# Kernel tuning notes

Hardware: AMD Instinct MI355X
Metric: run time of the kernel (lower is better)

Reference implementation:

```python
import jax, jax.numpy as jnp
import numpy as np

N_NODES = 100_000
N_EDGES = 3_200_000
NR = 10_000
NRHO = 10_000
CUTOFF = 6.0
RHO_MAX = 60.0


def natural_cubic_coeffs(x, y):
    """Natural cubic spline coefficients. x:[K], y:[K,C] -> a,b,c,d each [K-1,C]."""
    K, C = y.shape
    h = np.diff(x)
    rhs = 6.0 * ((y[2:] - y[1:-1]) / h[1:, None] - (y[1:-1] - y[:-2]) / h[:-1, None])
    n = K - 2
    diag = 2.0 * (h[:-1] + h[1:])
    off = h[1:-1]
    # Thomas algorithm for the tridiagonal system (natural BC: M[0]=M[K-1]=0)
    cp = np.zeros(n)
    dp = np.zeros((n, C))
    cp[0] = off[0] / diag[0] if n > 1 else 0.0
    dp[0] = rhs[0] / diag[0]
    for i in range(1, n):
        denom = diag[i] - off[i - 1] * cp[i - 1]
        if i < n - 1:
            cp[i] = off[i] / denom
        dp[i] = (rhs[i] - off[i - 1] * dp[i - 1]) / denom
    M = np.zeros((K, C))
    M[n] = dp[n - 1]
    for i in range(n - 2, -1, -1):
        M[i + 1] = dp[i] - cp[i] * M[i + 2]
    a = y[:-1]
    b = (y[1:] - y[:-1]) / h[:, None] - h[:, None] * (2.0 * M[:-1] + M[1:]) / 6.0
    c = M[:-1] / 2.0
    d = (M[1:] - M[:-1]) / (6.0 * h[:, None])
    f32 = lambda z: jnp.asarray(z, dtype=jnp.float32)
    return f32(a), f32(b), f32(c), f32(d)


def spline_eval(x, knots, a, b, c, d):
    """Piecewise cubic eval. x:[M], knots:[K], coeffs:[K-1,C] -> [M,C]."""
    idx = jnp.clip(jnp.searchsorted(knots, x, side='right') - 1, 0, knots.shape[0] - 2)
    s = (x - knots[idx])[:, None]  # offset within segment
    return a[idx] + s * (b[idx] + s * (c[idx] + s * d[idx]))


def setup_inputs() -> dict:
    key = jax.random.key(0)
    k1, k2, k3 = jax.random.split(key, 3)
    # edge displacement vectors; norms ~ chi(3)*1.2, well within cutoff
    r = jax.random.normal(k1, (N_EDGES, 3), dtype=jnp.float32) * 1.2
    src = jax.random.randint(k2, (N_EDGES,), 0, N_NODES, dtype=jnp.int32)
    dst = jax.random.randint(k3, (N_EDGES,), 0, N_NODES, dtype=jnp.int32)
    # synthetic smooth setfl tables (density, r*phi, embedding)
    rs = np.linspace(0.0, CUTOFF, NR)
    rhos_g = np.linspace(0.0, RHO_MAX, NRHO)
    density = np.exp(-rs)
    rphi = 27.2 * 0.529 * np.exp(-2.0 * rs) * (1.0 + 2.0 * rs)
    embedded = -np.sqrt(rhos_g) + 0.05 * rhos_g
    rad_a, rad_b, rad_c, rad_d = natural_cubic_coeffs(rs, np.stack([density, rphi], axis=1))
    emb_a, emb_b, emb_c, emb_d = natural_cubic_coeffs(rhos_g, embedded[:, None])
    return dict(
        r=r, src=src, dst=dst, n_nodes=N_NODES,
        rs=jnp.asarray(rs, jnp.float32), rhos=jnp.asarray(rhos_g, jnp.float32),
        rad_a=rad_a, rad_b=rad_b, rad_c=rad_c, rad_d=rad_d,
        emb_a=emb_a, emb_b=emb_b, emb_c=emb_c, emb_d=emb_d,
    )


def reference(r, src, dst, n_nodes, rs, rhos, rad_a, rad_b, rad_c, rad_d,
              emb_a, emb_b, emb_c, emb_d):
    def energy(r_):
        bl = jnp.linalg.norm(r_, axis=1)                       # [E]
        rp = spline_eval(bl, rs, rad_a, rad_b, rad_c, rad_d)   # [E,2]
        rho_e = rp[:, 0]
        phi_e = rp[:, 1] / bl                                  # rphi / r
        node_rho = jax.ops.segment_sum(rho_e, dst, num_segments=n_nodes)  # [N]
        F = spline_eval(node_rho, rhos, emb_a, emb_b, emb_c, emb_d)[:, 0]
        return jnp.sum(F) + 0.5 * jnp.sum(phi_e)

    E, dEdr = jax.value_and_grad(energy)(r)
    # r_ij = x_dst - x_src  =>  F_k = sum_{src=k} dE/dr - sum_{dst=k} dE/dr
    forces = (jax.ops.segment_sum(dEdr, src, num_segments=n_nodes)
              - jax.ops.segment_sum(dEdr, dst, num_segments=n_nodes))
    return E, forces
```

## Files before the change

### kernel.cpp

```cpp
#include <hip/hip_runtime.h>
#include <math.h>


static constexpr int SHIFT_P = 12;
static constexpr int NPP     = 4096;
static constexpr int PMAX    = 32;
static constexpr int GSTRIDE = 32;
static constexpr int KR      = 8;
static constexpr int KB      = 16;
static constexpr int CH1     = 4096;
static constexpr int CH3     = 2048;

static constexpr float QSCALE = 524288.0f;
static constexpr float QSTEP  = 1.0f / QSCALE;
static constexpr float FSCALE = 1024.0f;
static constexpr float FSTEP  = 1.0f / FSCALE;

__device__ __forceinline__ double block_reduce_d(double v) {
    #pragma unroll
    for (int off = 32; off > 0; off >>= 1)
        v += __shfl_down(v, off, 64);
    __shared__ double smem[16];
    const int lane = threadIdx.x & 63;
    const int wave = threadIdx.x >> 6;
    if (threadIdx.x < 16) smem[threadIdx.x] = 0.0;
    __syncthreads();
    if (lane == 0) smem[wave] = v;
    __syncthreads();
    if (wave == 0) {
        v = (lane < 16) ? smem[lane] : 0.0;
        #pragma unroll
        for (int off = 8; off > 0; off >>= 1)
            v += __shfl_down(v, off, 64);
    }
    return v;
}

__device__ __forceinline__ int clamp_idx(int i, int hi) {
    return i < 0 ? 0 : (i > hi ? hi : i);
}

__device__ __forceinline__ unsigned f2bf(float f) {
    unsigned u = __float_as_uint(f);
    return (u + 0x7FFFu + ((u >> 16) & 1u)) >> 16;
}
__device__ __forceinline__ float bf2f_hi(unsigned w) { return __uint_as_float(w & 0xFFFF0000u); }
__device__ __forceinline__ float bf2f_lo(unsigned w) { return __uint_as_float(w << 16); }
__device__ __forceinline__ unsigned fq(float f) {
    float s = f * FSCALE;
    s = fminf(fmaxf(s, -1.0e9f), 1.0e9f);
    return (unsigned)(int)rintf(s);
}

__global__ void eam_prep(
    const float* __restrict__ rad_a, const float* __restrict__ rad_b,
    const float* __restrict__ rad_c, const float* __restrict__ rad_d,
    const float* __restrict__ ea, const float* __restrict__ eb,
    const float* __restrict__ ec, const float* __restrict__ ed,
    float4* __restrict__ pack8, float4* __restrict__ pack4,
    int* __restrict__ gCur, int nr1, int nrho1)
{
    const int i = blockIdx.x * 256 + threadIdx.x;
    if (i < 2 * PMAX * GSTRIDE) gCur[i] = 0;
    if (i < nr1) {
        pack8[2*i]   = make_float4(rad_a[2*i], rad_a[2*i+1], rad_b[2*i], rad_b[2*i+1]);
        pack8[2*i+1] = make_float4(rad_c[2*i], rad_c[2*i+1], rad_d[2*i], rad_d[2*i+1]);
    }
    if (i < nrho1)
        pack4[i] = make_float4(ea[i], eb[i], ec[i], ed[i]);
}


__global__ void __launch_bounds__(512) eam_p1a(
    const float* __restrict__ r, const int* __restrict__ dst,
    const float4* __restrict__ pack8,
    unsigned* __restrict__ recR, int* __restrict__ gCurR, double* __restrict__ p1,
    float2* __restrict__ ebuf,
    int n_edges, float inv_h, float h, int kmax, int P, int capR)
{
    __shared__ int hist[PMAX], base[PMAX], cur[PMAX], gbase[PMAX];
    __shared__ int tot;
    __shared__ unsigned buf[CH1];
    __shared__ unsigned char pbk[CH1];
    const int tid = threadIdx.x;
    const int e0 = blockIdx.x * CH1;
    const int e1 = min(e0 + CH1, n_edges);
    double phi = 0.0;
    unsigned rec[8]; int pk[8]; bool val[8];
    if (tid < P) hist[tid] = 0;
    __syncthreads();
    #pragma unroll
    for (int k = 0; k < 8; ++k) {
        const int e = e0 + k * 512 + tid;
        val[k] = e < e1;
        rec[k] = 0; pk[k] = 0;
        if (val[k]) {
            const float x = r[3*e], y = r[3*e+1], z = r[3*e+2];
            const float bl = sqrtf(x*x + y*y + z*z);
            int idx = (int)(bl * inv_h); idx = idx > kmax ? kmax : idx;
            const float s = bl - (float)idx * h;
            const float4 q0 = pack8[2*idx];
            const float4 q1 = pack8[2*idx + 1];
            const float rho  = q0.x + s*(q0.z + s*(q1.x + s*q1.z));
            const float rphi = q0.y + s*(q0.w + s*(q1.y + s*q1.w));
            phi += 0.5 * (double)(rphi / bl);
            const float drho  = q0.z + s*(2.0f*q1.x + 3.0f*q1.z*s);
            const float drphi = q0.w + s*(2.0f*q1.y + 3.0f*q1.w*s);
            const float inv_bl = 1.0f / bl;
            const float dphi = (drphi - rphi * inv_bl) * inv_bl;
            ebuf[e] = make_float2(drho, dphi);
            const int node = dst[e];
            pk[k] = node >> SHIFT_P;
            int q = (int)(rho * QSCALE + 0.5f);
            q = q < 0 ? 0 : (q > 0xFFFFF ? 0xFFFFF : q);
            rec[k] = ((unsigned)(node & (NPP - 1)) << 20) | (unsigned)q;
            atomicAdd(&hist[pk[k]], 1);
        }
    }
    __syncthreads();
    if (tid < 64) {
        const int lane = tid;
        const int hv = (lane < P) ? hist[lane] : 0;
        int s = hv;
        #pragma unroll
        for (int off = 1; off < 32; off <<= 1) {
            const int t = __shfl_up(s, off, 64);
            if (lane >= off) s += t;
        }
        if (lane < P) {
            base[lane] = s - hv;
            cur[lane]  = s - hv;
            gbase[lane] = hv ? atomicAdd(&gCurR[lane * GSTRIDE], hv) : 0;
        }
        if (lane == P - 1) tot = s;
    }
    __syncthreads();
    #pragma unroll
    for (int k = 0; k < 8; ++k) {
        if (val[k]) {
            const int pos = atomicAdd(&cur[pk[k]], 1);
            buf[pos] = rec[k];
            pbk[pos] = (unsigned char)pk[k];
        }
    }
    __syncthreads();
    const int T = tot;
    for (int i = tid; i < T; i += 512) {
        const int pp = pbk[i];
        const int gi = gbase[pp] + (i - base[pp]);
        if (gi < capR) recR[(size_t)pp * capR + gi] = buf[i];
    }
    const double bs = block_reduce_d(phi);
    if (tid == 0) p1[blockIdx.x] = bs;
}

__global__ void __launch_bounds__(512) eam_p1b(
    const unsigned* __restrict__ recR, const int* __restrict__ gCurR,
    float* __restrict__ partR, int capR)
{
    __shared__ unsigned acc[NPP];
    const int tid = threadIdx.x;
    const int p = blockIdx.x / KR, j = blockIdx.x % KR;
    for (int i = tid; i < NPP; i += 512) acc[i] = 0u;
    __syncthreads();
    int cnt = gCurR[p * GSTRIDE]; cnt = cnt > capR ? capR : cnt;
    const int per = (((cnt + KR - 1) / KR) + 3) & ~3;
    const int lo = j * per, hi = min(lo + per, cnt);
    const unsigned* seg = recR + (size_t)p * capR;
    int i = lo + 4 * tid;
    for (; i + 4 * 512 + 3 < hi; i += 2 * 4 * 512) {
        const uint4 a = *(const uint4*)(seg + i);
        const uint4 b = *(const uint4*)(seg + i + 4 * 512);
        atomicAdd(&acc[a.x >> 20], a.x & 0xFFFFFu);
        atomicAdd(&acc[a.y >> 20], a.y & 0xFFFFFu);
        atomicAdd(&acc[a.z >> 20], a.z & 0xFFFFFu);
        atomicAdd(&acc[a.w >> 20], a.w & 0xFFFFFu);
        atomicAdd(&acc[b.x >> 20], b.x & 0xFFFFFu);
        atomicAdd(&acc[b.y >> 20], b.y & 0xFFFFFu);
        atomicAdd(&acc[b.z >> 20], b.z & 0xFFFFFu);
        atomicAdd(&acc[b.w >> 20], b.w & 0xFFFFFu);
    }
    for (; i + 3 < hi; i += 4 * 512) {
        const uint4 a = *(const uint4*)(seg + i);
        atomicAdd(&acc[a.x >> 20], a.x & 0xFFFFFu);
        atomicAdd(&acc[a.y >> 20], a.y & 0xFFFFFu);
        atomicAdd(&acc[a.z >> 20], a.z & 0xFFFFFu);
        atomicAdd(&acc[a.w >> 20], a.w & 0xFFFFFu);
    }
    for (int t = (hi & ~3) + tid; t < hi; t += 512) {
        const unsigned w = seg[t];
        atomicAdd(&acc[w >> 20], w & 0xFFFFFu);
    }
    __syncthreads();
    float* out = partR + (size_t)blockIdx.x * NPP;
    for (int k = tid; k < NPP; k += 512) out[k] = (float)acc[k] * QSTEP;
}

__global__ void __launch_bounds__(1024) eam_p1c(
    const float* __restrict__ partR, const float4* __restrict__ pack4,
    float* __restrict__ Fp, double* __restrict__ p2,
    int n_nodes, float inv_h, float h, int kmax)
{
    const int n = blockIdx.x * 1024 + threadIdx.x;
    double fsum = 0.0;
    if (n < n_nodes) {
        const int p = n >> SHIFT_P, l = n & (NPP - 1);
        float rho = 0.0f;
        #pragma unroll
        for (int j = 0; j < KR; ++j)
            rho += partR[(size_t)(p * KR + j) * NPP + l];
        int idx = clamp_idx((int)(rho * inv_h), kmax);
        const float s = rho - (float)idx * h;
        const float4 q = pack4[idx];
        fsum = (double)(q.x + s*(q.y + s*(q.z + s*q.w)));
        Fp[n] = q.y + s*(2.0f*q.z + 3.0f*q.w*s);
    }
    const double bs = block_reduce_d(fsum);
    if (threadIdx.x == 0) p2[blockIdx.x] = bs;
}


__global__ void __launch_bounds__(512) eam_p3a(
    const float* __restrict__ r, const int* __restrict__ src, const int* __restrict__ dst,
    const float2* __restrict__ ebuf, const float* __restrict__ Fp,
    int2* __restrict__ recF, int* __restrict__ gCurF,
    int n_edges, int P, int capF)
{
    __shared__ int hist[PMAX], base[PMAX], cur[PMAX], gbase[PMAX];
    __shared__ int tot;
    __shared__ int2 buf[2 * CH3];
    __shared__ unsigned char pbk[2 * CH3];
    const int tid = threadIdx.x;
    const int e0 = blockIdx.x * CH3;
    const int e1 = min(e0 + CH3, n_edges);
    int2 sa[4], da[4]; int ps[4], pd[4]; bool val[4];
    if (tid < P) hist[tid] = 0;
    __syncthreads();
    #pragma unroll
    for (int k = 0; k < 4; ++k) {
        const int e = e0 + k * 512 + tid;
        val[k] = e < e1;
        ps[k] = pd[k] = 0;
        sa[k] = da[k] = make_int2(0, 0);
        if (val[k]) {
            const float x = r[3*e], y = r[3*e+1], z = r[3*e+2];
            const float bl = sqrtf(x*x + y*y + z*z);
            const float inv_bl = 1.0f / bl;
            const float2 dd = ebuf[e];
            const int si = src[e], di = dst[e];
            const float g = Fp[di] * dd.x + 0.5f * dd.y;
            const float coef = g * inv_bl;
            const unsigned bx = f2bf(coef * x), by = f2bf(coef * y), bz = f2bf(coef * z);
            ps[k] = si >> SHIFT_P;
            pd[k] = di >> SHIFT_P;
            sa[k] = make_int2((int)(((unsigned)(si & (NPP-1)) << 16) | bx),
                              (int)((by << 16) | bz));
            da[k] = make_int2((int)(((unsigned)(di & (NPP-1)) << 16) | (bx ^ 0x8000u)),
                              (int)(((by ^ 0x8000u) << 16) | (bz ^ 0x8000u)));
            atomicAdd(&hist[ps[k]], 1);
            atomicAdd(&hist[pd[k]], 1);
        }
    }
    __syncthreads();
    if (tid < 64) {
        const int lane = tid;
        const int hv = (lane < P) ? hist[lane] : 0;
        int s = hv;
        #pragma unroll
        for (int off = 1; off < 32; off <<= 1) {
            const int t = __shfl_up(s, off, 64);
            if (lane >= off) s += t;
        }
        if (lane < P) {
            base[lane] = s - hv;
            cur[lane]  = s - hv;
            gbase[lane] = hv ? atomicAdd(&gCurF[lane * GSTRIDE], hv) : 0;
        }
        if (lane == P - 1) tot = s;
    }
    __syncthreads();
    #pragma unroll
    for (int k = 0; k < 4; ++k) {
        if (val[k]) {
            int pos = atomicAdd(&cur[ps[k]], 1);
            buf[pos] = sa[k];
            pbk[pos] = (unsigned char)ps[k];
            pos = atomicAdd(&cur[pd[k]], 1);
            buf[pos] = da[k];
            pbk[pos] = (unsigned char)pd[k];
        }
    }
    __syncthreads();
    const int T = tot;
    for (int i = tid; i < T; i += 512) {
        const int pp = pbk[i];
        const int gi = gbase[pp] + (i - base[pp]);
        if (gi < capF) recF[(size_t)pp * capF + gi] = buf[i];
    }
}

__global__ void __launch_bounds__(512) eam_p3b(
    const int2* __restrict__ recF, const int* __restrict__ gCurF,
    int* __restrict__ partF, int capF)
{
    __shared__ unsigned acc[NPP * 3];
    const int tid = threadIdx.x;
    const int p = blockIdx.x / KB, j = blockIdx.x % KB;
    for (int i = tid; i < NPP * 3; i += 512) acc[i] = 0u;
    __syncthreads();
    int cnt = gCurF[p * GSTRIDE]; cnt = cnt > capF ? capF : cnt;
    const int per = (((cnt + KB - 1) / KB) + 3) & ~3;
    const int lo = j * per, hi = min(lo + per, cnt);
    const int2* seg = recF + (size_t)p * capF;
    int i = lo + 2 * tid;
    for (; i + 6 * 512 + 1 < hi; i += 8 * 512) {
        const uint4 a = *(const uint4*)(seg + i);
        const uint4 b = *(const uint4*)(seg + i + 2 * 512);
        const uint4 c = *(const uint4*)(seg + i + 4 * 512);
        const uint4 d = *(const uint4*)(seg + i + 6 * 512);
        int li;
        li = (int)(a.x >> 16) * 3;
        atomicAdd(&acc[li+0], fq(bf2f_lo(a.x))); atomicAdd(&acc[li+1], fq(bf2f_hi(a.y))); atomicAdd(&acc[li+2], fq(bf2f_lo(a.y)));
        li = (int)(a.z >> 16) * 3;
        atomicAdd(&acc[li+0], fq(bf2f_lo(a.z))); atomicAdd(&acc[li+1], fq(bf2f_hi(a.w))); atomicAdd(&acc[li+2], fq(bf2f_lo(a.w)));
        li = (int)(b.x >> 16) * 3;
        atomicAdd(&acc[li+0], fq(bf2f_lo(b.x))); atomicAdd(&acc[li+1], fq(bf2f_hi(b.y))); atomicAdd(&acc[li+2], fq(bf2f_lo(b.y)));
        li = (int)(b.z >> 16) * 3;
        atomicAdd(&acc[li+0], fq(bf2f_lo(b.z))); atomicAdd(&acc[li+1], fq(bf2f_hi(b.w))); atomicAdd(&acc[li+2], fq(bf2f_lo(b.w)));
        li = (int)(c.x >> 16) * 3;
        atomicAdd(&acc[li+0], fq(bf2f_lo(c.x))); atomicAdd(&acc[li+1], fq(bf2f_hi(c.y))); atomicAdd(&acc[li+2], fq(bf2f_lo(c.y)));
        li = (int)(c.z >> 16) * 3;
        atomicAdd(&acc[li+0], fq(bf2f_lo(c.z))); atomicAdd(&acc[li+1], fq(bf2f_hi(c.w))); atomicAdd(&acc[li+2], fq(bf2f_lo(c.w)));
        li = (int)(d.x >> 16) * 3;
        atomicAdd(&acc[li+0], fq(bf2f_lo(d.x))); atomicAdd(&acc[li+1], fq(bf2f_hi(d.y))); atomicAdd(&acc[li+2], fq(bf2f_lo(d.y)));
        li = (int)(d.z >> 16) * 3;
        atomicAdd(&acc[li+0], fq(bf2f_lo(d.z))); atomicAdd(&acc[li+1], fq(bf2f_hi(d.w))); atomicAdd(&acc[li+2], fq(bf2f_lo(d.w)));
    }
    for (; i + 1 < hi; i += 2 * 512) {
        const uint4 a = *(const uint4*)(seg + i);
        int li = (int)(a.x >> 16) * 3;
        atomicAdd(&acc[li+0], fq(bf2f_lo(a.x))); atomicAdd(&acc[li+1], fq(bf2f_hi(a.y))); atomicAdd(&acc[li+2], fq(bf2f_lo(a.y)));
        li = (int)(a.z >> 16) * 3;
        atomicAdd(&acc[li+0], fq(bf2f_lo(a.z))); atomicAdd(&acc[li+1], fq(bf2f_hi(a.w))); atomicAdd(&acc[li+2], fq(bf2f_lo(a.w)));
    }
    for (int t = (hi & ~1) + tid; t < hi; t += 512) {
        const int2 rc = seg[t];
        const unsigned w0 = (unsigned)rc.x, w1 = (unsigned)rc.y;
        const int li = (int)(w0 >> 16) * 3;
        atomicAdd(&acc[li+0], fq(bf2f_lo(w0)));
        atomicAdd(&acc[li+1], fq(bf2f_hi(w1)));
        atomicAdd(&acc[li+2], fq(bf2f_lo(w1)));
    }
    __syncthreads();
    int* out = partF + (size_t)blockIdx.x * (NPP * 3);
    for (int k = tid; k < NPP * 3; k += 512) out[k] = (int)acc[k];
}

__global__ void __launch_bounds__(1024) eam_p3c(
    const int* __restrict__ partF, float* __restrict__ outF, int n_nodes)
{
    const int g = blockIdx.x * 1024 + threadIdx.x;
    if (g >= 3 * n_nodes) return;
    const int n = g / 3, c = g - 3 * n;
    const int p = n >> SHIFT_P, l = n & (NPP - 1);
    int v = 0;
    #pragma unroll
    for (int j = 0; j < KB; ++j)
        v += partF[(size_t)(p * KB + j) * (NPP * 3) + l * 3 + c];
    outF[g] = (float)v * FSTEP;
}

__global__ void __launch_bounds__(256) eam_final_e(
    const double* __restrict__ p1, int n1,
    const double* __restrict__ p2, int n2,
    float* __restrict__ outE)
{
    double v = 0.0;
    for (int i = threadIdx.x; i < n1; i += 256) v += p1[i];
    for (int i = threadIdx.x; i < n2; i += 256) v += p2[i];
    const double bs = block_reduce_d(v);
    if (threadIdx.x == 0) *outE = (float)bs;
}


__global__ void __launch_bounds__(256) eam_pass1(
    const float* __restrict__ r, const int* __restrict__ dst,
    const float* __restrict__ rs,
    const float* __restrict__ rad_a, const float* __restrict__ rad_b,
    const float* __restrict__ rad_c, const float* __restrict__ rad_d,
    float* __restrict__ node_rho, double* __restrict__ p1,
    int n_edges, float inv_h, int kmax)
{
    const int e = blockIdx.x * 256 + threadIdx.x;
    double phi_half = 0.0;
    if (e < n_edges) {
        const float x = r[3*e], y = r[3*e+1], z = r[3*e+2];
        const float bl = sqrtf(x*x + y*y + z*z);
        const int idx = clamp_idx((int)(bl * inv_h), kmax);
        const float s = bl - rs[idx];
        const float a0 = rad_a[2*idx], a1 = rad_a[2*idx+1];
        const float b0 = rad_b[2*idx], b1 = rad_b[2*idx+1];
        const float c0 = rad_c[2*idx], c1 = rad_c[2*idx+1];
        const float d0 = rad_d[2*idx], d1 = rad_d[2*idx+1];
        const float rho  = a0 + s*(b0 + s*(c0 + s*d0));
        const float rphi = a1 + s*(b1 + s*(c1 + s*d1));
        unsafeAtomicAdd(&node_rho[dst[e]], rho);
        phi_half = 0.5 * (double)(rphi / bl);
    }
    const double bs = block_reduce_d(phi_half);
    if (threadIdx.x == 0) p1[blockIdx.x] = bs;
}

__global__ void __launch_bounds__(256) eam_pass2(
    const float* __restrict__ node_rho, const float* __restrict__ rhos,
    const float* __restrict__ ea, const float* __restrict__ eb,
    const float* __restrict__ ec, const float* __restrict__ ed,
    float* __restrict__ Fp, double* __restrict__ p2,
    int n_nodes, float inv_h, int kmax)
{
    const int n = blockIdx.x * 256 + threadIdx.x;
    double fsum = 0.0;
    if (n < n_nodes) {
        const float rho = node_rho[n];
        const int idx = clamp_idx((int)(rho * inv_h), kmax);
        const float s = rho - rhos[idx];
        const float A = ea[idx], B = eb[idx], C = ec[idx], D = ed[idx];
        fsum = (double)(A + s*(B + s*(C + s*D)));
        Fp[n] = B + s*(2.0f*C + 3.0f*D*s);
    }
    const double bs = block_reduce_d(fsum);
    if (threadIdx.x == 0) p2[blockIdx.x] = bs;
}

__global__ void __launch_bounds__(256) eam_pass3(
    const float* __restrict__ r, const int* __restrict__ src,
    const int* __restrict__ dst, const float* __restrict__ rs,
    const float* __restrict__ rad_a, const float* __restrict__ rad_b,
    const float* __restrict__ rad_c, const float* __restrict__ rad_d,
    const float* __restrict__ Fp, float* __restrict__ forces,
    int n_edges, float inv_h, int kmax)
{
    const int e = blockIdx.x * 256 + threadIdx.x;
    if (e >= n_edges) return;
    const float x = r[3*e], y = r[3*e+1], z = r[3*e+2];
    const float bl = sqrtf(x*x + y*y + z*z);
    const int idx = clamp_idx((int)(bl * inv_h), kmax);
    const float s = bl - rs[idx];
    const float a1 = rad_a[2*idx+1];
    const float b0 = rad_b[2*idx], b1 = rad_b[2*idx+1];
    const float c0 = rad_c[2*idx], c1 = rad_c[2*idx+1];
    const float d0 = rad_d[2*idx], d1 = rad_d[2*idx+1];
    const float drho  = b0 + s*(2.0f*c0 + 3.0f*d0*s);
    const float rphi  = a1 + s*(b1 + s*(c1 + s*d1));
    const float drphi = b1 + s*(2.0f*c1 + 3.0f*d1*s);
    const float inv_bl = 1.0f / bl;
    const float dphi = (drphi - rphi*inv_bl) * inv_bl;
    const int si = src[e], di = dst[e];
    const float g = Fp[di]*drho + 0.5f*dphi;
    const float coef = g * inv_bl;
    const float fx = coef*x, fy = coef*y, fz = coef*z;
    unsafeAtomicAdd(&forces[3*si+0], fx);
    unsafeAtomicAdd(&forces[3*si+1], fy);
    unsafeAtomicAdd(&forces[3*si+2], fz);
    unsafeAtomicAdd(&forces[3*di+0], -fx);
    unsafeAtomicAdd(&forces[3*di+1], -fy);
    unsafeAtomicAdd(&forces[3*di+2], -fz);
}


extern "C" void kernel_launch(void* const* d_in, const int* in_sizes, int n_in,
                              void* d_out, int out_size, void* d_ws, size_t ws_size,
                              hipStream_t stream) {
    const float* r     = (const float*)d_in[0];
    const int*   src   = (const int*)d_in[1];
    const int*   dst   = (const int*)d_in[2];
    const float* rs    = (const float*)d_in[4];
    const float* rhos  = (const float*)d_in[5];
    const float* rad_a = (const float*)d_in[6];
    const float* rad_b = (const float*)d_in[7];
    const float* rad_c = (const float*)d_in[8];
    const float* rad_d = (const float*)d_in[9];
    const float* ea    = (const float*)d_in[10];
    const float* eb    = (const float*)d_in[11];
    const float* ec    = (const float*)d_in[12];
    const float* ed    = (const float*)d_in[13];

    const int n_edges = in_sizes[0] / 3;
    const int n_nodes = (out_size - 1) / 3;
    const int nr      = in_sizes[4];
    const int nrho    = in_sizes[5];

    float* outE = (float*)d_out;
    float* outF = (float*)d_out + 1;

    const float inv_hr   = (float)((double)(nr - 1) / 6.0);
    const float hr       = (float)(6.0 / (double)(nr - 1));
    const float inv_hrho = (float)((double)(nrho - 1) / 60.0);
    const float hrho     = (float)(60.0 / (double)(nrho - 1));

    auto al = [](size_t x) { return (x + 255) & ~(size_t)255; };
    char* ws = (char*)d_ws;

    const int P    = (n_nodes + NPP - 1) >> SHIFT_P;
    const int nb1a = (n_edges + CH1 - 1) / CH1;
    const int nb3a = (n_edges + CH3 - 1) / CH3;
    const int nb1c = (n_nodes + 1023) / 1024;
    const int nb3c = (3 * n_nodes + 1023) / 1024;
    const int capR = (n_edges / P + n_edges / (8 * P) + 2048) & ~3;
    const int capF = (2 * n_edges / P + n_edges / (4 * P) + 4096) & ~3;

    size_t off = 0;
    float4*   pack8 = (float4*)(ws + off);   off += al((size_t)(nr - 1) * 32);
    float4*   pack4 = (float4*)(ws + off);   off += al((size_t)(nrho - 1) * 16);
    int*      gCur  = (int*)(ws + off);      off += al((size_t)2 * PMAX * GSTRIDE * 4);
    float*    Fp    = (float*)(ws + off);    off += al((size_t)n_nodes * 4);
    double*   p1b   = (double*)(ws + off);   off += al((size_t)nb1a * 8);
    double*   p2b   = (double*)(ws + off);   off += al((size_t)nb1c * 8);
    float2*   ebuf  = (float2*)(ws + off);   off += al((size_t)n_edges * 8);
    float*    partR = (float*)(ws + off);    off += al((size_t)P * KR * NPP * 4);
    int*      partF = (int*)(ws + off);      off += al((size_t)P * KB * NPP * 12);
    unsigned* recR  = (unsigned*)(ws + off); off += al((size_t)P * capR * 4);
    int2*     recF  = (int2*)(ws + off);     off += al((size_t)P * capF * 8);
    const size_t need = off;

    if (P <= PMAX && ws_size >= need) {
        int* gCurR = gCur;
        int* gCurF = gCur + PMAX * GSTRIDE;
        const int npk = (nr - 1) > (nrho - 1) ? (nr - 1) : (nrho - 1);
        eam_prep<<<(npk + 255) / 256, 256, 0, stream>>>(
            rad_a, rad_b, rad_c, rad_d, ea, eb, ec, ed, pack8, pack4, gCur, nr - 1, nrho - 1);
        eam_p1a<<<nb1a, 512, 0, stream>>>(
            r, dst, pack8, recR, gCurR, p1b, ebuf, n_edges, inv_hr, hr, nr - 2, P, capR);
        eam_p1b<<<P * KR, 512, 0, stream>>>(recR, gCurR, partR, capR);
        eam_p1c<<<nb1c, 1024, 0, stream>>>(
            partR, pack4, Fp, p2b, n_nodes, inv_hrho, hrho, nrho - 2);
        eam_p3a<<<nb3a, 512, 0, stream>>>(
            r, src, dst, ebuf, Fp, recF, gCurF, n_edges, P, capF);
        eam_p3b<<<P * KB, 512, 0, stream>>>(recF, gCurF, partF, capF);
        eam_p3c<<<nb3c, 1024, 0, stream>>>(partF, outF, n_nodes);
        eam_final_e<<<1, 256, 0, stream>>>(p1b, nb1a, p2b, nb1c, outE);
    } else {
        size_t o = 0;
        float* node_rho = (float*)(ws + o); o += al((size_t)n_nodes * 4);
        float* Fp2      = (float*)(ws + o); o += al((size_t)n_nodes * 4);
        const int nb_e = (n_edges + 255) / 256;
        const int nb_n = (n_nodes + 255) / 256;
        double* p1 = (double*)(ws + o); o += al((size_t)nb_e * 8);
        double* p2 = (double*)(ws + o);
        hipMemsetAsync(d_out, 0, (size_t)out_size * sizeof(float), stream);
        hipMemsetAsync(node_rho, 0, (size_t)n_nodes * sizeof(float), stream);
        eam_pass1<<<nb_e, 256, 0, stream>>>(r, dst, rs, rad_a, rad_b, rad_c, rad_d,
                                            node_rho, p1, n_edges, inv_hr, nr - 2);
        eam_pass2<<<nb_n, 256, 0, stream>>>(node_rho, rhos, ea, eb, ec, ed,
                                            Fp2, p2, n_nodes, inv_hrho, nrho - 2);
        eam_final_e<<<1, 256, 0, stream>>>(p1, nb_e, p2, nb_n, outE);
        eam_pass3<<<nb_e, 256, 0, stream>>>(r, src, dst, rs, rad_a, rad_b, rad_c, rad_d,
                                            Fp2, outF, n_edges, inv_hr, nr - 2);
    }
}
```

Before: 230.6 us.

## Replace binned quantized density scatter with replicated global float atomics

```diff
diff --git a/kernel.cpp b/kernel.cpp
--- a/kernel.cpp
+++ b/kernel.cpp
@@ -6,13 +6,10 @@
 static constexpr int NPP     = 4096;
 static constexpr int PMAX    = 32;
 static constexpr int GSTRIDE = 32;
-static constexpr int KR      = 8;
 static constexpr int KB      = 16;
-static constexpr int CH1     = 4096;
 static constexpr int CH3     = 2048;
-
-static constexpr float QSCALE = 524288.0f;
-static constexpr float QSTEP  = 1.0f / QSCALE;
+static constexpr int NCPY    = 8;
+
 static constexpr float FSCALE = 1024.0f;
 static constexpr float FSTEP  = 1.0f / FSCALE;
 
@@ -71,144 +68,48 @@
 }
 
 
-__global__ void __launch_bounds__(512) eam_p1a(
+__global__ void __launch_bounds__(256) eam_p1a(
     const float* __restrict__ r, const int* __restrict__ dst,
     const float4* __restrict__ pack8,
-    unsigned* __restrict__ recR, int* __restrict__ gCurR, double* __restrict__ p1,
-    float2* __restrict__ ebuf,
-    int n_edges, float inv_h, float h, int kmax, int P, int capR)
-{
-    __shared__ int hist[PMAX], base[PMAX], cur[PMAX], gbase[PMAX];
-    __shared__ int tot;
-    __shared__ unsigned buf[CH1];
-    __shared__ unsigned char pbk[CH1];
-    const int tid = threadIdx.x;
-    const int e0 = blockIdx.x * CH1;
-    const int e1 = min(e0 + CH1, n_edges);
+    float* __restrict__ rho8, float2* __restrict__ ebuf, double* __restrict__ p1,
+    int n_edges, int n_nodes, float inv_h, float h, int kmax)
+{
+    const int e = blockIdx.x * 256 + threadIdx.x;
     double phi = 0.0;
-    unsigned rec[8]; int pk[8]; bool val[8];
-    if (tid < P) hist[tid] = 0;
-    __syncthreads();
-    #pragma unroll
-    for (int k = 0; k < 8; ++k) {
-        const int e = e0 + k * 512 + tid;
-        val[k] = e < e1;
-        rec[k] = 0; pk[k] = 0;
-        if (val[k]) {
-            const float x = r[3*e], y = r[3*e+1], z = r[3*e+2];
-            const float bl = sqrtf(x*x + y*y + z*z);
-            int idx = (int)(bl * inv_h); idx = idx > kmax ? kmax : idx;
-            const float s = bl - (float)idx * h;
-            const float4 q0 = pack8[2*idx];
-            const float4 q1 = pack8[2*idx + 1];
-            const float rho  = q0.x + s*(q0.z + s*(q1.x + s*q1.z));
-            const float rphi = q0.y + s*(q0.w + s*(q1.y + s*q1.w));
-            phi += 0.5 * (double)(rphi / bl);
-            const float drho  = q0.z + s*(2.0f*q1.x + 3.0f*q1.z*s);
-            const float drphi = q0.w + s*(2.0f*q1.y + 3.0f*q1.w*s);
-            const float inv_bl = 1.0f / bl;
-            const float dphi = (drphi - rphi * inv_bl) * inv_bl;
-            ebuf[e] = make_float2(drho, dphi);
-            const int node = dst[e];
-            pk[k] = node >> SHIFT_P;
-            int q = (int)(rho * QSCALE + 0.5f);
-            q = q < 0 ? 0 : (q > 0xFFFFF ? 0xFFFFF : q);
-            rec[k] = ((unsigned)(node & (NPP - 1)) << 20) | (unsigned)q;
-            atomicAdd(&hist[pk[k]], 1);
-        }
-    }
-    __syncthreads();
-    if (tid < 64) {
-        const int lane = tid;
-        const int hv = (lane < P) ? hist[lane] : 0;
-        int s = hv;
-        #pragma unroll
-        for (int off = 1; off < 32; off <<= 1) {
-            const int t = __shfl_up(s, off, 64);
-            if (lane >= off) s += t;
-        }
-        if (lane < P) {
-            base[lane] = s - hv;
-            cur[lane]  = s - hv;
-            gbase[lane] = hv ? atomicAdd(&gCurR[lane * GSTRIDE], hv) : 0;
-        }
-        if (lane == P - 1) tot = s;
-    }
-    __syncthreads();
-    #pragma unroll
-    for (int k = 0; k < 8; ++k) {
-        if (val[k]) {
-            const int pos = atomicAdd(&cur[pk[k]], 1);
-            buf[pos] = rec[k];
-            pbk[pos] = (unsigned char)pk[k];
-        }
-    }
-    __syncthreads();
-    const int T = tot;
-    for (int i = tid; i < T; i += 512) {
-        const int pp = pbk[i];
-        const int gi = gbase[pp] + (i - base[pp]);
-        if (gi < capR) recR[(size_t)pp * capR + gi] = buf[i];
+    if (e < n_edges) {
+        const float x = r[3*e], y = r[3*e+1], z = r[3*e+2];
+        const float bl = sqrtf(x*x + y*y + z*z);
+        int idx = (int)(bl * inv_h); idx = idx > kmax ? kmax : idx;
+        const float s = bl - (float)idx * h;
+        const float4 q0 = pack8[2*idx];
+        const float4 q1 = pack8[2*idx + 1];
+        const float rho  = q0.x + s*(q0.z + s*(q1.x + s*q1.z));
+        const float rphi = q0.y + s*(q0.w + s*(q1.y + s*q1.w));
+        phi = 0.5 * (double)(rphi / bl);
+        const float drho  = q0.z + s*(2.0f*q1.x + 3.0f*q1.z*s);
+        const float drphi = q0.w + s*(2.0f*q1.y + 3.0f*q1.w*s);
+        const float inv_bl = 1.0f / bl;
+        const float dphi = (drphi - rphi * inv_bl) * inv_bl;
+        ebuf[e] = make_float2(drho, dphi);
+        float* dstp = rho8 + (size_t)(blockIdx.x & (NCPY - 1)) * n_nodes + dst[e];
+        unsafeAtomicAdd(dstp, rho);
     }
     const double bs = block_reduce_d(phi);
-    if (tid == 0) p1[blockIdx.x] = bs;
-}
-
-__global__ void __launch_bounds__(512) eam_p1b(
-    const unsigned* __restrict__ recR, const int* __restrict__ gCurR,
-    float* __restrict__ partR, int capR)
-{
-    __shared__ unsigned acc[NPP];
-    const int tid = threadIdx.x;
-    const int p = blockIdx.x / KR, j = blockIdx.x % KR;
-    for (int i = tid; i < NPP; i += 512) acc[i] = 0u;
-    __syncthreads();
-    int cnt = gCurR[p * GSTRIDE]; cnt = cnt > capR ? capR : cnt;
-    const int per = (((cnt + KR - 1) / KR) + 3) & ~3;
-    const int lo = j * per, hi = min(lo + per, cnt);
-    const unsigned* seg = recR + (size_t)p * capR;
-    int i = lo + 4 * tid;
-    for (; i + 4 * 512 + 3 < hi; i += 2 * 4 * 512) {
-        const uint4 a = *(const uint4*)(seg + i);
-        const uint4 b = *(const uint4*)(seg + i + 4 * 512);
-        atomicAdd(&acc[a.x >> 20], a.x & 0xFFFFFu);
-        atomicAdd(&acc[a.y >> 20], a.y & 0xFFFFFu);
-        atomicAdd(&acc[a.z >> 20], a.z & 0xFFFFFu);
-        atomicAdd(&acc[a.w >> 20], a.w & 0xFFFFFu);
-        atomicAdd(&acc[b.x >> 20], b.x & 0xFFFFFu);
-        atomicAdd(&acc[b.y >> 20], b.y & 0xFFFFFu);
-        atomicAdd(&acc[b.z >> 20], b.z & 0xFFFFFu);
-        atomicAdd(&acc[b.w >> 20], b.w & 0xFFFFFu);
-    }
-    for (; i + 3 < hi; i += 4 * 512) {
-        const uint4 a = *(const uint4*)(seg + i);
-        atomicAdd(&acc[a.x >> 20], a.x & 0xFFFFFu);
-        atomicAdd(&acc[a.y >> 20], a.y & 0xFFFFFu);
-        atomicAdd(&acc[a.z >> 20], a.z & 0xFFFFFu);
-        atomicAdd(&acc[a.w >> 20], a.w & 0xFFFFFu);
-    }
-    for (int t = (hi & ~3) + tid; t < hi; t += 512) {
-        const unsigned w = seg[t];
-        atomicAdd(&acc[w >> 20], w & 0xFFFFFu);
-    }
-    __syncthreads();
-    float* out = partR + (size_t)blockIdx.x * NPP;
-    for (int k = tid; k < NPP; k += 512) out[k] = (float)acc[k] * QSTEP;
+    if (threadIdx.x == 0) p1[blockIdx.x] = bs;
 }
 
 __global__ void __launch_bounds__(1024) eam_p1c(
-    const float* __restrict__ partR, const float4* __restrict__ pack4,
+    const float* __restrict__ rho8, const float4* __restrict__ pack4,
     float* __restrict__ Fp, double* __restrict__ p2,
     int n_nodes, float inv_h, float h, int kmax)
 {
     const int n = blockIdx.x * 1024 + threadIdx.x;
     double fsum = 0.0;
     if (n < n_nodes) {
-        const int p = n >> SHIFT_P, l = n & (NPP - 1);
         float rho = 0.0f;
         #pragma unroll
-        for (int j = 0; j < KR; ++j)
-            rho += partR[(size_t)(p * KR + j) * NPP + l];
+        for (int j = 0; j < NCPY; ++j)
+            rho += rho8[(size_t)j * n_nodes + n];
         int idx = clamp_idx((int)(rho * inv_h), kmax);
         const float s = rho - (float)idx * h;
         const float4 q = pack4[idx];
@@ -502,11 +403,10 @@
     char* ws = (char*)d_ws;
 
     const int P    = (n_nodes + NPP - 1) >> SHIFT_P;
-    const int nb1a = (n_edges + CH1 - 1) / CH1;
+    const int nb1a = (n_edges + 255) / 256;
     const int nb3a = (n_edges + CH3 - 1) / CH3;
     const int nb1c = (n_nodes + 1023) / 1024;
     const int nb3c = (3 * n_nodes + 1023) / 1024;
-    const int capR = (n_edges / P + n_edges / (8 * P) + 2048) & ~3;
     const int capF = (2 * n_edges / P + n_edges / (4 * P) + 4096) & ~3;
 
     size_t off = 0;
@@ -517,23 +417,21 @@
     double*   p1b   = (double*)(ws + off);   off += al((size_t)nb1a * 8);
     double*   p2b   = (double*)(ws + off);   off += al((size_t)nb1c * 8);
     float2*   ebuf  = (float2*)(ws + off);   off += al((size_t)n_edges * 8);
-    float*    partR = (float*)(ws + off);    off += al((size_t)P * KR * NPP * 4);
+    float*    rho8  = (float*)(ws + off);    off += al((size_t)NCPY * n_nodes * 4);
     int*      partF = (int*)(ws + off);      off += al((size_t)P * KB * NPP * 12);
-    unsigned* recR  = (unsigned*)(ws + off); off += al((size_t)P * capR * 4);
     int2*     recF  = (int2*)(ws + off);     off += al((size_t)P * capF * 8);
     const size_t need = off;
 
     if (P <= PMAX && ws_size >= need) {
-        int* gCurR = gCur;
         int* gCurF = gCur + PMAX * GSTRIDE;
         const int npk = (nr - 1) > (nrho - 1) ? (nr - 1) : (nrho - 1);
+        hipMemsetAsync(rho8, 0, (size_t)NCPY * n_nodes * 4, stream);
         eam_prep<<<(npk + 255) / 256, 256, 0, stream>>>(
             rad_a, rad_b, rad_c, rad_d, ea, eb, ec, ed, pack8, pack4, gCur, nr - 1, nrho - 1);
-        eam_p1a<<<nb1a, 512, 0, stream>>>(
-            r, dst, pack8, recR, gCurR, p1b, ebuf, n_edges, inv_hr, hr, nr - 2, P, capR);
-        eam_p1b<<<P * KR, 512, 0, stream>>>(recR, gCurR, partR, capR);
+        eam_p1a<<<nb1a, 256, 0, stream>>>(
+            r, dst, pack8, rho8, ebuf, p1b, n_edges, n_nodes, inv_hr, hr, nr - 2);
         eam_p1c<<<nb1c, 1024, 0, stream>>>(
-            partR, pack4, Fp, p2b, n_nodes, inv_hrho, hrho, nrho - 2);
+            rho8, pack4, Fp, p2b, n_nodes, inv_hrho, hrho, nrho - 2);
         eam_p3a<<<nb3a, 512, 0, stream>>>(
             r, src, dst, ebuf, Fp, recF, gCurF, n_edges, P, capF);
         eam_p3b<<<P * KB, 512, 0, stream>>>(recF, gCurF, partF, capF);
```

New measurement: 350.8 us. 52.2% more time.
